# Kernel tuning notes

Measured on AMD Instinct MI355X. Metric: run time of the kernel, lower is better.

Reference implementation:

```python
import jax, jax.numpy as jnp
import numpy as np

PAD = 0  # padding_index
BIG = 10000.0

B, S = 1024, 128
V, E, H, T = 200, 512, 512, 24


def setup_inputs() -> dict:
    key = jax.random.key(0)
    ks = jax.random.split(key, 12)
    sequences = jax.random.randint(ks[0], (B, S), 0, V, dtype=jnp.int32)
    labels = jax.random.randint(ks[1], (B, S), 0, T, dtype=jnp.int32)
    true_lengths = jax.random.randint(ks[2], (B,), 1, S, dtype=jnp.int32)
    emb = jax.random.normal(ks[3], (V, E), dtype=jnp.float32) * 0.1
    emb = emb.at[PAD].set(0.0)  # nn.Embedding padding_idx zeros that row
    w1 = jax.random.normal(ks[4], (H, H), dtype=jnp.float32) * (1.0 / np.sqrt(H))
    b1 = jax.random.normal(ks[5], (H,), dtype=jnp.float32) * 0.01
    w2 = jax.random.normal(ks[6], (T, H), dtype=jnp.float32) * (1.0 / np.sqrt(H))
    b2 = jax.random.normal(ks[7], (T,), dtype=jnp.float32) * 0.01
    start_trans = jax.random.uniform(ks[8], (T,), jnp.float32, -0.1, 0.1)
    end_trans = jax.random.uniform(ks[9], (T,), jnp.float32, -0.1, 0.1)
    transitions = jax.random.uniform(ks[10], (T, T), jnp.float32, -0.1, 0.1)
    return {"sequences": sequences, "labels": labels, "true_lengths": true_lengths,
            "emb": emb, "w1": w1, "b1": b1, "w2": w2, "b2": b2,
            "start_trans": start_trans, "end_trans": end_trans, "transitions": transitions}


def _emissions(sequences, emb, w1, b1, w2, b2):
    pad_mask = (sequences == PAD).astype(jnp.float32)  # [B,S]
    x = emb[sequences]                                  # [B,S,E]
    h = jax.nn.relu(x @ w1.T + b1)                      # [B,S,H]
    scores = jax.nn.relu(h @ w2.T + b2)                 # [B,S,T]
    scores = scores.at[:, :, PAD].add(pad_mask * BIG)
    return scores


def _crf_nll_mean(emissions, labels, start_trans, end_trans, transitions):
    # emissions [B,S,T], labels [B,S]; mask = all ones (none passed in forward)
    # numerator: score of gold path
    em_gold = jnp.take_along_axis(emissions, labels[..., None], axis=2)[..., 0]  # [B,S]
    num = (start_trans[labels[:, 0]]
           + em_gold.sum(axis=1)
           + transitions[labels[:, :-1], labels[:, 1:]].sum(axis=1)
           + end_trans[labels[:, -1]])  # [B]
    # denominator: forward algorithm via scan over time
    em_t = jnp.swapaxes(emissions, 0, 1)  # [S,B,T]
    alpha0 = start_trans[None, :] + em_t[0]  # [B,T]

    def step(alpha, emit):
        # alpha [B,T_prev], transitions [T_prev,T_next], emit [B,T_next]
        nxt = jax.nn.logsumexp(alpha[:, :, None] + transitions[None] + emit[:, None, :], axis=1)
        return nxt, None

    alpha, _ = jax.lax.scan(step, alpha0, em_t[1:])
    denom = jax.nn.logsumexp(alpha + end_trans[None, :], axis=1)  # [B]
    llh = num - denom
    return -jnp.mean(llh)


def reference(sequences, labels, true_lengths, emb, w1, b1, w2, b2,
              start_trans, end_trans, transitions):
    emissions = _emissions(sequences, emb, w1, b1, w2, b2)
    return _crf_nll_mean(emissions, labels, start_trans, end_trans, transitions)
```

## Files before the change

### kernel.cpp

```cpp
#include <hip/hip_runtime.h>
#include <math.h>

#define PAD_IDX 0
#define BIGV 10000.0f
constexpr int B_ = 1024, S_ = 128, V_ = 200, E_ = 512, H_ = 512, T_ = 24;

constexpr int OFF_H  = 262144;
constexpr int OFF_EM = 364544;
constexpr int OFF_W  = 369344;
constexpr int OFF_MX = 374144;
constexpr int OFF_GP = 374344;

typedef __attribute__((ext_vector_type(8)))  short    bf8frag;
typedef __attribute__((ext_vector_type(16))) float    facc16;
typedef __attribute__((ext_vector_type(4)))  unsigned u32x4;

__device__ __forceinline__ unsigned short f2bf(float f) {
    unsigned u = __float_as_uint(f);
    u += 0x7fffu + ((u >> 16) & 1u);
    return (unsigned short)(u >> 16);
}
__device__ __forceinline__ unsigned pkbf(float lo, float hi) {
    const unsigned a = __float_as_uint(lo), b = __float_as_uint(hi);
    return ((a + 0x8000u) >> 16) | ((b + 0x8000u) & 0xffff0000u);
}

__global__ __launch_bounds__(256) void transpose_kernel(
    const float* __restrict__ w1, unsigned short* __restrict__ w1Tb,
    float* __restrict__ out)
{
    __shared__ float tile[64][65];
    const int bi = blockIdx.x >> 3, bj = blockIdx.x & 7;
    const int tx = threadIdx.x & 63, r0 = (threadIdx.x >> 6) * 16;
    if (blockIdx.x == 0 && threadIdx.x == 0) out[0] = 0.f;
    #pragma unroll
    for (int m = 0; m < 16; ++m) {
        const int r = r0 + m;
        tile[r][tx] = w1[(size_t)(bi * 64 + r) * 512 + bj * 64 + tx];
    }
    __syncthreads();
    #pragma unroll
    for (int m = 0; m < 16; ++m) {
        const int r = r0 + m;
        w1Tb[(size_t)(bj * 64 + r) * 512 + bi * 64 + tx] = f2bf(tile[tx][r]);
    }
}

__global__ __launch_bounds__(256) void h_kernel(
    const float* __restrict__ emb, const unsigned short* __restrict__ w1Tb,
    const float* __restrict__ b1, float* __restrict__ h_ws)
{
    __shared__ float xi[2 * E_];
    __shared__ float part_s[4][64][8];
    const int pair = blockIdx.x >> 1, half = blockIdx.x & 1;
    const int v0 = pair * 2, v1 = v0 + 1;
    const int tid = threadIdx.x;
    {
        const float* __restrict__ x0 = emb + (size_t)v0 * E_;
        const float* __restrict__ x1 = emb + (size_t)v1 * E_;
        #pragma unroll
        for (int m = 0; m < 2; ++m) {
            const int k = tid + m * 256;
            xi[2 * k]     = x0[k];
            xi[2 * k + 1] = x1[k];
        }
    }
    __syncthreads();
    const int part = tid >> 6, quad = tid & 63;
    const int t0 = half * 256 + quad * 4, k0 = part * 128;
    float a0 = 0.f, a1 = 0.f, a2 = 0.f, a3 = 0.f;
    float c0 = 0.f, c1 = 0.f, c2 = 0.f, c3 = 0.f;
    const unsigned short* __restrict__ wp = w1Tb + (size_t)k0 * H_ + t0;
    const float2* __restrict__ xp = (const float2*)xi + k0;
    #pragma unroll 4
    for (int i = 0; i < 128; ++i) {
        const uint2 wu = *(const uint2*)(wp + (size_t)i * H_);
        const float2 x = xp[i];
        const float w0 = __uint_as_float(wu.x << 16);
        const float w1v = __uint_as_float(wu.x & 0xffff0000u);
        const float w2v = __uint_as_float(wu.y << 16);
        const float w3v = __uint_as_float(wu.y & 0xffff0000u);
        a0 = fmaf(w0,  x.x, a0); a1 = fmaf(w1v, x.x, a1);
        a2 = fmaf(w2v, x.x, a2); a3 = fmaf(w3v, x.x, a3);
        c0 = fmaf(w0,  x.y, c0); c1 = fmaf(w1v, x.y, c1);
        c2 = fmaf(w2v, x.y, c2); c3 = fmaf(w3v, x.y, c3);
    }
    part_s[part][quad][0] = a0; part_s[part][quad][1] = a1;
    part_s[part][quad][2] = a2; part_s[part][quad][3] = a3;
    part_s[part][quad][4] = c0; part_s[part][quad][5] = c1;
    part_s[part][quad][6] = c2; part_s[part][quad][7] = c3;
    __syncthreads();
    {
        const int q2 = tid >> 2, r0 = tid & 3;
        const float s0 = (part_s[0][q2][r0]     + part_s[1][q2][r0])
                       + (part_s[2][q2][r0]     + part_s[3][q2][r0]);
        const float s1 = (part_s[0][q2][r0 + 4] + part_s[1][q2][r0 + 4])
                       + (part_s[2][q2][r0 + 4] + part_s[3][q2][r0 + 4]);
        const int t = half * 256 + tid;
        const float bb = b1[t];
        h_ws[(size_t)v0 * H_ + t] = fmaxf(s0 + bb, 0.f);
        h_ws[(size_t)v1 * H_ + t] = fmaxf(s1 + bb, 0.f);
    }
}

__global__ __launch_bounds__(256) void emis_kernel(
    const float* __restrict__ h_ws, const float* __restrict__ w2,
    const float* __restrict__ b2, float* __restrict__ em_table,
    float* __restrict__ w_table, float* __restrict__ emax_arr)
{
    __shared__ float em_row[32];
    const int v = blockIdx.x;
    const int t = threadIdx.x;
    const int wave = t >> 6, lane = t & 63;
    const float* __restrict__ hrow = h_ws + (size_t)v * H_;
    for (int jj2 = 0; jj2 < 6; ++jj2) {
        const int jo = wave * 6 + jj2;
        float part = 0.f;
        #pragma unroll
        for (int m = 0; m < H_ / 64; ++m) {
            const int k = lane + m * 64;
            part = fmaf(hrow[k], w2[(size_t)jo * H_ + k], part);
        }
        #pragma unroll
        for (int off = 32; off; off >>= 1)
            part += __shfl_xor(part, off, 64);
        if (lane == 0) {
            float val = fmaxf(part + b2[jo], 0.f);
            if (v == 0 && jo == PAD_IDX) val += BIGV;
            em_row[jo] = val;
        }
    }
    __syncthreads();
    if (t < 32) {
        float x = (t < T_) ? em_row[t] : -INFINITY;
        float mx = x;
        #pragma unroll
        for (int off = 16; off; off >>= 1)
            mx = fmaxf(mx, __shfl_xor(mx, off, 32));
        if (t < T_) {
            em_table[v * T_ + t] = x;
            w_table[v * T_ + t]  = __expf(x - mx);
        }
        if (t == 0) emax_arr[v] = mx;
    }
}

__global__ __launch_bounds__(256) void gold_kernel(
    const int* __restrict__ seq, const int* __restrict__ labels,
    const float* __restrict__ start_t, const float* __restrict__ end_t,
    const float* __restrict__ trans, const float* __restrict__ em_table,
    const float* __restrict__ emax_arr, float* __restrict__ gp_ws)
{
    const int grp = threadIdx.x >> 5, j = threadIdx.x & 31;
    const int b = blockIdx.x * 8 + grp;
    const int* __restrict__ srow = seq + (size_t)b * S_;
    const int* __restrict__ lrow = labels + (size_t)b * S_;
    float gp = 0.f;
    #pragma unroll
    for (int r = 0; r < 4; ++r) {
        const int s = j + r * 32;
        const int tk = srow[s], ls = lrow[s];
        gp += em_table[tk * T_ + ls];
        if (s >= 1) gp -= emax_arr[tk];
        if (s < S_ - 1) gp += trans[ls * T_ + lrow[s + 1]];
        if (s == 0) gp += start_t[ls];
        if (s == S_ - 1) gp += end_t[ls];
    }
    #pragma unroll
    for (int off = 16; off; off >>= 1)
        gp += __shfl_xor(gp, off, 32);
    if (j == 0) gp_ws[b] = gp;
}

__global__ __launch_bounds__(128) void crf_kernel(
    const int* __restrict__ seq,
    const float* __restrict__ start_t, const float* __restrict__ end_t,
    const float* __restrict__ trans, const float* __restrict__ em_table,
    const float* __restrict__ w_table, const float* __restrict__ gp_ws,
    float* __restrict__ out)
{
    __shared__ __align__(16) float w_s[V_ * T_];
    __shared__ int   tok_s[S_ * 32];
    __shared__ float meet_s[64 * 12];
    __shared__ float logb_s[64];
    const int tid = threadIdx.x;
    const int g = blockIdx.x;

    for (int i = tid; i < V_ * T_ / 4; i += 128)
        ((float4*)w_s)[i] = ((const float4*)w_table)[i];
    {
        const int bq = tid & 31, c = tid >> 5;
        const int* __restrict__ src = seq + (size_t)(g * 32 + bq) * S_ + c * 32;
        #pragma unroll 4
        for (int i = 0; i < 32; ++i)
            tok_s[(c * 32 + i) * 32 + bq] = src[i];
    }
    __syncthreads();

    const bool isF = (tid < 64);
    const int lane = tid & 63;
    const int n = lane & 31;
    const int h = lane >> 5;

    u32x4 A1p, A2p;
    {
        float a1e[8], a2e[8];
        #pragma unroll
        for (int j = 0; j < 8; ++j) {
            const int k1 = 8 * h + j;
            const int k2 = 16 + 8 * h + j;
            float v1 = 0.f, v2 = 0.f;
            if (n < T_) {
                v1 = __expf(isF ? trans[k1 * T_ + n] : trans[n * T_ + k1]);
                if (k2 < T_)
                    v2 = __expf(isF ? trans[k2 * T_ + n] : trans[n * T_ + k2]);
            }
            a1e[j] = v1; a2e[j] = v2;
        }
        #pragma unroll
        for (int r = 0; r < 4; ++r) {
            A1p[r] = pkbf(a1e[2 * r], a1e[2 * r + 1]);
            A2p[r] = pkbf(a2e[2 * r], a2e[2 * r + 1]);
        }
    }

    float logacc;
    u32x4 B1p, B2p;
    {
        const int tokI = tok_s[(isF ? 0 : (S_ - 1)) * 32 + n];
        float q1[8], q2[8];
        if (isF) {
            float e1[8], e2[8];
            #pragma unroll
            for (int j = 0; j < 8; ++j) { e1[j] = 0.f; e2[j] = 0.f; }
            float mx = -INFINITY;
            #pragma unroll
            for (int j = 0; j < 8; ++j) {
                const int r1 = 8 * h + j;
                e1[j] = start_t[r1] + em_table[tokI * T_ + r1];
                mx = fmaxf(mx, e1[j]);
            }
            if (h == 0) {
                #pragma unroll
                for (int j = 0; j < 8; ++j) {
                    const int r2 = 16 + j;
                    e2[j] = start_t[r2] + em_table[tokI * T_ + r2];
                    mx = fmaxf(mx, e2[j]);
                }
            }
            mx = fmaxf(mx, __shfl_xor(mx, 32, 64));
            #pragma unroll
            for (int j = 0; j < 8; ++j) {
                q1[j] = __expf(e1[j] - mx);
                q2[j] = (h == 0) ? __expf(e2[j] - mx) : 0.f;
            }
            logacc = mx;
        } else {
            #pragma unroll
            for (int j = 0; j < 8; ++j) {
                const int r1 = 8 * h + j;
                q1[j] = w_s[tokI * T_ + r1] * __expf(end_t[r1]);
                const int r2 = 16 + j;
                q2[j] = (h == 0) ? w_s[tokI * T_ + r2] * __expf(end_t[r2]) : 0.f;
            }
            logacc = 0.f;
        }
        #pragma unroll
        for (int r = 0; r < 4; ++r) {
            B1p[r] = pkbf(q1[2 * r], q1[2 * r + 1]);
            B2p[r] = pkbf(q2[2 * r], q2[2 * r + 1]);
        }
    }

    const int dir  = isF ? 1 : -1;
    const int offi = isF ? 1 : (S_ - 2);

    float4 Wc0, Wc1, Wc2;
    {
        const int tk = tok_s[offi * 32 + n];
        const float* wb = w_s + tk * T_ + 4 * h;
        Wc0 = *(const float4*)(wb);
        Wc1 = *(const float4*)(wb + 8);
        Wc2 = *(const float4*)(wb + 16);
    }

    float d[12];
    for (int s = 1; s <= 63; ++s) {
        const int sn = (s < 63) ? (s + 1) : 63;
        const int tkN = tok_s[(offi + dir * (sn - 1)) * 32 + n];
        const float* wbn = w_s + tkN * T_ + 4 * h;
        const float4 Wn0 = *(const float4*)(wbn);
        const float4 Wn1 = *(const float4*)(wbn + 8);
        const float4 Wn2 = *(const float4*)(wbn + 16);

        facc16 acc;
        #pragma unroll
        for (int r = 0; r < 16; ++r) acc[r] = 0.f;
        acc = __builtin_amdgcn_mfma_f32_32x32x16_bf16(
                  __builtin_bit_cast(bf8frag, A2p),
                  __builtin_bit_cast(bf8frag, B2p), acc, 0, 0, 0);
        acc = __builtin_amdgcn_mfma_f32_32x32x16_bf16(
                  __builtin_bit_cast(bf8frag, A1p),
                  __builtin_bit_cast(bf8frag, B1p), acc, 0, 0, 0);

        d[0] = acc[0]*Wc0.x;  d[1] = acc[1]*Wc0.y;  d[2]  = acc[2]*Wc0.z;  d[3]  = acc[3]*Wc0.w;
        d[4] = acc[4]*Wc1.x;  d[5] = acc[5]*Wc1.y;  d[6]  = acc[6]*Wc1.z;  d[7]  = acc[7]*Wc1.w;
        d[8] = acc[8]*Wc2.x;  d[9] = acc[9]*Wc2.y;  d[10] = acc[10]*Wc2.z; d[11] = acc[11]*Wc2.w;

        if ((s & 15) == 0 || s == 63) {
            float mx = d[0];
            #pragma unroll
            for (int r = 1; r < 12; ++r) mx = fmaxf(mx, d[r]);
            mx = fmaxf(mx, __shfl_xor(mx, 32, 64));
            const float inv = 1.0f / mx;
            #pragma unroll
            for (int r = 0; r < 12; ++r) d[r] *= inv;
            logacc += __logf(mx);
        }

        const unsigned P0 = pkbf(d[0], d[1]),  P1 = pkbf(d[2], d[3]);
        const unsigned P2 = pkbf(d[4], d[5]),  P3 = pkbf(d[6], d[7]);
        const unsigned P4 = pkbf(d[8], d[9]),  P5 = pkbf(d[10], d[11]);
        const unsigned XP0 = (unsigned)__shfl_xor((int)P0, 32, 64);
        const unsigned XP1 = (unsigned)__shfl_xor((int)P1, 32, 64);
        const unsigned XP2 = (unsigned)__shfl_xor((int)P2, 32, 64);
        const unsigned XP3 = (unsigned)__shfl_xor((int)P3, 32, 64);
        const unsigned XP4 = (unsigned)__shfl_xor((int)P4, 32, 64);
        const unsigned XP5 = (unsigned)__shfl_xor((int)P5, 32, 64);
        B1p[0] = h ? XP2 : P0;  B1p[1] = h ? XP3 : P1;
        B1p[2] = h ? P2  : XP0; B1p[3] = h ? P3  : XP1;
        B2p[0] = h ? 0u  : P4;  B2p[1] = h ? 0u  : P5;
        B2p[2] = h ? 0u  : XP4; B2p[3] = h ? 0u  : XP5;

        Wc0 = Wn0; Wc1 = Wn1; Wc2 = Wn2;
    }

    if (!isF) {
        #pragma unroll
        for (int r = 0; r < 12; ++r) meet_s[lane * 12 + r] = d[r];
        logb_s[lane] = logacc;
    }
    __syncthreads();
    if (isF) {
        facc16 acc;
        #pragma unroll
        for (int r = 0; r < 16; ++r) acc[r] = 0.f;
        acc = __builtin_amdgcn_mfma_f32_32x32x16_bf16(
                  __builtin_bit_cast(bf8frag, A2p),
                  __builtin_bit_cast(bf8frag, B2p), acc, 0, 0, 0);
        acc = __builtin_amdgcn_mfma_f32_32x32x16_bf16(
                  __builtin_bit_cast(bf8frag, A1p),
                  __builtin_bit_cast(bf8frag, B1p), acc, 0, 0, 0);
        float dot = 0.f;
        #pragma unroll
        for (int r = 0; r < 12; ++r)
            dot = fmaf(acc[r], meet_s[lane * 12 + r], dot);
        dot += __shfl_xor(dot, 32, 64);
        const float denom = logacc + logb_s[lane] + __logf(dot);
        float val = 0.f;
        if (h == 0)
            val = (denom - gp_ws[g * 32 + n]) * (1.0f / (float)B_);
        #pragma unroll
        for (int off = 32; off; off >>= 1)
            val += __shfl_xor(val, off, 64);
        if (lane == 0) atomicAdd(out, val);
    }
}

extern "C" void kernel_launch(void* const* d_in, const int* in_sizes, int n_in,
                              void* d_out, int out_size, void* d_ws, size_t ws_size,
                              hipStream_t stream) {
    const int*   seq     = (const int*)d_in[0];
    const int*   labels  = (const int*)d_in[1];
    const float* emb     = (const float*)d_in[3];
    const float* w1      = (const float*)d_in[4];
    const float* b1      = (const float*)d_in[5];
    const float* w2      = (const float*)d_in[6];
    const float* b2      = (const float*)d_in[7];
    const float* start_t = (const float*)d_in[8];
    const float* end_t   = (const float*)d_in[9];
    const float* trans   = (const float*)d_in[10];

    float* ws       = (float*)d_ws;
    unsigned short* w1Tb = (unsigned short*)d_ws;
    float* h_ws     = ws + OFF_H;
    float* em_table = ws + OFF_EM;
    float* w_table  = ws + OFF_W;
    float* emax_arr = ws + OFF_MX;
    float* gp_ws    = ws + OFF_GP;
    float* out      = (float*)d_out;

    transpose_kernel<<<64, 256, 0, stream>>>(w1, w1Tb, out);
    h_kernel<<<200, 256, 0, stream>>>(emb, w1Tb, b1, h_ws);
    emis_kernel<<<V_, 256, 0, stream>>>(h_ws, w2, b2, em_table, w_table, emax_arr);
    gold_kernel<<<B_ / 8, 256, 0, stream>>>(seq, labels, start_t, end_t, trans,
                                            em_table, emax_arr, gp_ws);
    crf_kernel<<<B_ / 32, 128, 0, stream>>>(seq, start_t, end_t, trans,
                                            em_table, w_table, gp_ws, out);
}
```

Measured before the change: 119.6 us.

## Fuse MLP kernels and merge gold-path scoring into CRF kernel

Merges the hidden-layer and emission kernels into one mlp_kernel, where each block handles two vocab rows and keeps h in shared memory instead of a global workspace. The gold-path score kernel becomes two extra waves inside the CRF kernel: they accumulate per-sequence scores into shared memory with atomics while the forward/backward waves run their recurrence. This cuts the launch count from five to three and drops the global round trips for h and the gold scores. In exchange the MLP phase runs on half as many blocks with longer per-block loops, and correctness depends on the __syncthreads calls in the two divergent branches pairing up.

```diff
diff --git a/kernel.cpp b/kernel.cpp
--- a/kernel.cpp
+++ b/kernel.cpp
@@ -5,11 +5,9 @@
 #define BIGV 10000.0f
 constexpr int B_ = 1024, S_ = 128, V_ = 200, E_ = 512, H_ = 512, T_ = 24;
 
-constexpr int OFF_H  = 262144;
-constexpr int OFF_EM = 364544;
-constexpr int OFF_W  = 369344;
-constexpr int OFF_MX = 374144;
-constexpr int OFF_GP = 374344;
+constexpr int OFF_EM = 262144;
+constexpr int OFF_W  = 267008;
+constexpr int OFF_MX = 271872;
 
 typedef __attribute__((ext_vector_type(8)))  short    bf8frag;
 typedef __attribute__((ext_vector_type(16))) float    facc16;
@@ -46,15 +44,19 @@
     }
 }
 
-__global__ __launch_bounds__(256) void h_kernel(
+__global__ __launch_bounds__(256) void mlp_kernel(
     const float* __restrict__ emb, const unsigned short* __restrict__ w1Tb,
-    const float* __restrict__ b1, float* __restrict__ h_ws)
+    const float* __restrict__ b1, const float* __restrict__ w2,
+    const float* __restrict__ b2, float* __restrict__ em_table,
+    float* __restrict__ w_table, float* __restrict__ emax_arr)
 {
     __shared__ float xi[2 * E_];
-    __shared__ float part_s[4][64][8];
-    const int pair = blockIdx.x >> 1, half = blockIdx.x & 1;
-    const int v0 = pair * 2, v1 = v0 + 1;
+    __shared__ float part_s[2][128][8];
+    __shared__ float hs[2][H_];
+    __shared__ float em_row[2][32];
+    const int v0 = blockIdx.x * 2, v1 = v0 + 1;
     const int tid = threadIdx.x;
+
     {
         const float* __restrict__ x0 = emb + (size_t)v0 * E_;
         const float* __restrict__ x1 = emb + (size_t)v1 * E_;
@@ -66,304 +68,303 @@
         }
     }
     __syncthreads();
-    const int part = tid >> 6, quad = tid & 63;
-    const int t0 = half * 256 + quad * 4, k0 = part * 128;
-    float a0 = 0.f, a1 = 0.f, a2 = 0.f, a3 = 0.f;
-    float c0 = 0.f, c1 = 0.f, c2 = 0.f, c3 = 0.f;
-    const unsigned short* __restrict__ wp = w1Tb + (size_t)k0 * H_ + t0;
-    const float2* __restrict__ xp = (const float2*)xi + k0;
-    #pragma unroll 4
-    for (int i = 0; i < 128; ++i) {
-        const uint2 wu = *(const uint2*)(wp + (size_t)i * H_);
-        const float2 x = xp[i];
-        const float w0 = __uint_as_float(wu.x << 16);
-        const float w1v = __uint_as_float(wu.x & 0xffff0000u);
-        const float w2v = __uint_as_float(wu.y << 16);
-        const float w3v = __uint_as_float(wu.y & 0xffff0000u);
-        a0 = fmaf(w0,  x.x, a0); a1 = fmaf(w1v, x.x, a1);
-        a2 = fmaf(w2v, x.x, a2); a3 = fmaf(w3v, x.x, a3);
-        c0 = fmaf(w0,  x.y, c0); c1 = fmaf(w1v, x.y, c1);
-        c2 = fmaf(w2v, x.y, c2); c3 = fmaf(w3v, x.y, c3);
-    }
-    part_s[part][quad][0] = a0; part_s[part][quad][1] = a1;
-    part_s[part][quad][2] = a2; part_s[part][quad][3] = a3;
-    part_s[part][quad][4] = c0; part_s[part][quad][5] = c1;
-    part_s[part][quad][6] = c2; part_s[part][quad][7] = c3;
-    __syncthreads();
-    {
-        const int q2 = tid >> 2, r0 = tid & 3;
-        const float s0 = (part_s[0][q2][r0]     + part_s[1][q2][r0])
-                       + (part_s[2][q2][r0]     + part_s[3][q2][r0]);
-        const float s1 = (part_s[0][q2][r0 + 4] + part_s[1][q2][r0 + 4])
-                       + (part_s[2][q2][r0 + 4] + part_s[3][q2][r0 + 4]);
-        const int t = half * 256 + tid;
-        const float bb = b1[t];
-        h_ws[(size_t)v0 * H_ + t] = fmaxf(s0 + bb, 0.f);
-        h_ws[(size_t)v1 * H_ + t] = fmaxf(s1 + bb, 0.f);
-    }
-}
-
-__global__ __launch_bounds__(256) void emis_kernel(
-    const float* __restrict__ h_ws, const float* __restrict__ w2,
-    const float* __restrict__ b2, float* __restrict__ em_table,
-    float* __restrict__ w_table, float* __restrict__ emax_arr)
-{
-    __shared__ float em_row[32];
-    const int v = blockIdx.x;
-    const int t = threadIdx.x;
-    const int wave = t >> 6, lane = t & 63;
-    const float* __restrict__ hrow = h_ws + (size_t)v * H_;
-    for (int jj2 = 0; jj2 < 6; ++jj2) {
-        const int jo = wave * 6 + jj2;
-        float part = 0.f;
+
+    {
+        const int part = tid >> 7;
+        const int tq   = tid & 127;
+        const int t0 = tq * 4, k0 = part * 256;
+        float a0 = 0.f, a1 = 0.f, a2 = 0.f, a3 = 0.f;
+        float c0 = 0.f, c1 = 0.f, c2 = 0.f, c3 = 0.f;
+        const unsigned short* __restrict__ wp = w1Tb + (size_t)k0 * H_ + t0;
+        const float2* __restrict__ xp = (const float2*)xi + k0;
+        #pragma unroll 4
+        for (int i = 0; i < 256; ++i) {
+            const uint2 wu = *(const uint2*)(wp + (size_t)i * H_);
+            const float2 x = xp[i];
+            const float w0 = __uint_as_float(wu.x << 16);
+            const float w1v = __uint_as_float(wu.x & 0xffff0000u);
+            const float w2v = __uint_as_float(wu.y << 16);
+            const float w3v = __uint_as_float(wu.y & 0xffff0000u);
+            a0 = fmaf(w0,  x.x, a0); a1 = fmaf(w1v, x.x, a1);
+            a2 = fmaf(w2v, x.x, a2); a3 = fmaf(w3v, x.x, a3);
+            c0 = fmaf(w0,  x.y, c0); c1 = fmaf(w1v, x.y, c1);
+            c2 = fmaf(w2v, x.y, c2); c3 = fmaf(w3v, x.y, c3);
+        }
+        part_s[part][tq][0] = a0; part_s[part][tq][1] = a1;
+        part_s[part][tq][2] = a2; part_s[part][tq][3] = a3;
+        part_s[part][tq][4] = c0; part_s[part][tq][5] = c1;
+        part_s[part][tq][6] = c2; part_s[part][tq][7] = c3;
+    }
+    __syncthreads();
+    {
         #pragma unroll
-        for (int m = 0; m < H_ / 64; ++m) {
-            const int k = lane + m * 64;
-            part = fmaf(hrow[k], w2[(size_t)jo * H_ + k], part);
-        }
-        #pragma unroll
-        for (int off = 32; off; off >>= 1)
-            part += __shfl_xor(part, off, 64);
-        if (lane == 0) {
-            float val = fmaxf(part + b2[jo], 0.f);
-            if (v == 0 && jo == PAD_IDX) val += BIGV;
-            em_row[jo] = val;
-        }
-    }
-    __syncthreads();
-    if (t < 32) {
-        float x = (t < T_) ? em_row[t] : -INFINITY;
+        for (int m = 0; m < 2; ++m) {
+            const int t = tid + m * 256;
+            const int q2 = t >> 2, r = t & 3;
+            const float s0 = part_s[0][q2][r]     + part_s[1][q2][r];
+            const float s1 = part_s[0][q2][r + 4] + part_s[1][q2][r + 4];
+            const float bb = b1[t];
+            hs[0][t] = fmaxf(s0 + bb, 0.f);
+            hs[1][t] = fmaxf(s1 + bb, 0.f);
+        }
+    }
+    __syncthreads();
+
+    {
+        const int wave = tid >> 6, lane = tid & 63;
+        const int vsel = wave >> 1;
+        const float* __restrict__ hrow = hs[vsel];
+        for (int jj2 = 0; jj2 < 12; ++jj2) {
+            const int j = (wave & 1) * 12 + jj2;
+            float part = 0.f;
+            #pragma unroll
+            for (int m = 0; m < H_ / 64; ++m) {
+                const int k = lane + m * 64;
+                part = fmaf(hrow[k], w2[(size_t)j * H_ + k], part);
+            }
+            #pragma unroll
+            for (int off = 32; off; off >>= 1)
+                part += __shfl_xor(part, off, 64);
+            if (lane == 0) {
+                float val = fmaxf(part + b2[j], 0.f);
+                if (v0 == 0 && vsel == 0 && j == PAD_IDX) val += BIGV;
+                em_row[vsel][j] = val;
+            }
+        }
+    }
+    __syncthreads();
+
+    if (tid < 64) {
+        const int grp = tid >> 5, j = tid & 31;
+        const int v = v0 + grp;
+        float x = (j < T_) ? em_row[grp][j] : -INFINITY;
         float mx = x;
         #pragma unroll
         for (int off = 16; off; off >>= 1)
             mx = fmaxf(mx, __shfl_xor(mx, off, 32));
-        if (t < T_) {
-            em_table[v * T_ + t] = x;
-            w_table[v * T_ + t]  = __expf(x - mx);
-        }
-        if (t == 0) emax_arr[v] = mx;
-    }
-}
-
-__global__ __launch_bounds__(256) void gold_kernel(
+        if (j < T_) {
+            em_table[v * T_ + j] = x;
+            w_table[v * T_ + j]  = __expf(x - mx);
+        }
+        if (j == 0) emax_arr[v] = mx;
+    }
+}
+
+__global__ __launch_bounds__(256) void crf_kernel(
     const int* __restrict__ seq, const int* __restrict__ labels,
     const float* __restrict__ start_t, const float* __restrict__ end_t,
     const float* __restrict__ trans, const float* __restrict__ em_table,
-    const float* __restrict__ emax_arr, float* __restrict__ gp_ws)
-{
-    const int grp = threadIdx.x >> 5, j = threadIdx.x & 31;
-    const int b = blockIdx.x * 8 + grp;
-    const int* __restrict__ srow = seq + (size_t)b * S_;
-    const int* __restrict__ lrow = labels + (size_t)b * S_;
-    float gp = 0.f;
-    #pragma unroll
-    for (int r = 0; r < 4; ++r) {
-        const int s = j + r * 32;
-        const int tk = srow[s], ls = lrow[s];
-        gp += em_table[tk * T_ + ls];
-        if (s >= 1) gp -= emax_arr[tk];
-        if (s < S_ - 1) gp += trans[ls * T_ + lrow[s + 1]];
-        if (s == 0) gp += start_t[ls];
-        if (s == S_ - 1) gp += end_t[ls];
-    }
-    #pragma unroll
-    for (int off = 16; off; off >>= 1)
-        gp += __shfl_xor(gp, off, 32);
-    if (j == 0) gp_ws[b] = gp;
-}
-
-__global__ __launch_bounds__(128) void crf_kernel(
-    const int* __restrict__ seq,
-    const float* __restrict__ start_t, const float* __restrict__ end_t,
-    const float* __restrict__ trans, const float* __restrict__ em_table,
-    const float* __restrict__ w_table, const float* __restrict__ gp_ws,
+    const float* __restrict__ w_table, const float* __restrict__ emax_arr,
     float* __restrict__ out)
 {
     __shared__ __align__(16) float w_s[V_ * T_];
     __shared__ int   tok_s[S_ * 32];
     __shared__ float meet_s[64 * 12];
     __shared__ float logb_s[64];
+    __shared__ float gp_s[32];
     const int tid = threadIdx.x;
     const int g = blockIdx.x;
 
-    for (int i = tid; i < V_ * T_ / 4; i += 128)
+    for (int i = tid; i < V_ * T_ / 4; i += 256)
         ((float4*)w_s)[i] = ((const float4*)w_table)[i];
     {
         const int bq = tid & 31, c = tid >> 5;
-        const int* __restrict__ src = seq + (size_t)(g * 32 + bq) * S_ + c * 32;
-        #pragma unroll 4
-        for (int i = 0; i < 32; ++i)
-            tok_s[(c * 32 + i) * 32 + bq] = src[i];
-    }
-    __syncthreads();
-
-    const bool isF = (tid < 64);
-    const int lane = tid & 63;
-    const int n = lane & 31;
-    const int h = lane >> 5;
-
-    u32x4 A1p, A2p;
-    {
-        float a1e[8], a2e[8];
+        const int* __restrict__ src = seq + (size_t)(g * 32 + bq) * S_ + c * 16;
         #pragma unroll
-        for (int j = 0; j < 8; ++j) {
-            const int k1 = 8 * h + j;
-            const int k2 = 16 + 8 * h + j;
-            float v1 = 0.f, v2 = 0.f;
-            if (n < T_) {
-                v1 = __expf(isF ? trans[k1 * T_ + n] : trans[n * T_ + k1]);
-                if (k2 < T_)
-                    v2 = __expf(isF ? trans[k2 * T_ + n] : trans[n * T_ + k2]);
-            }
-            a1e[j] = v1; a2e[j] = v2;
-        }
-        #pragma unroll
-        for (int r = 0; r < 4; ++r) {
-            A1p[r] = pkbf(a1e[2 * r], a1e[2 * r + 1]);
-            A2p[r] = pkbf(a2e[2 * r], a2e[2 * r + 1]);
-        }
-    }
-
-    float logacc;
-    u32x4 B1p, B2p;
-    {
-        const int tokI = tok_s[(isF ? 0 : (S_ - 1)) * 32 + n];
-        float q1[8], q2[8];
+        for (int i = 0; i < 16; ++i)
+            tok_s[(c * 16 + i) * 32 + bq] = src[i];
+    }
+    if (tid < 32) gp_s[tid] = 0.f;
+    __syncthreads();
+
+    if (tid < 128) {
+        const bool isF = (tid < 64);
+        const int lane = tid & 63;
+        const int n = lane & 31;
+        const int h = lane >> 5;
+
+        u32x4 A1p, A2p;
+        {
+            float a1e[8], a2e[8];
+            #pragma unroll
+            for (int j = 0; j < 8; ++j) {
+                const int k1 = 8 * h + j;
+                const int k2 = 16 + 8 * h + j;
+                float v1 = 0.f, v2 = 0.f;
+                if (n < T_) {
+                    v1 = __expf(isF ? trans[k1 * T_ + n] : trans[n * T_ + k1]);
+                    if (k2 < T_)
+                        v2 = __expf(isF ? trans[k2 * T_ + n] : trans[n * T_ + k2]);
+                }
+                a1e[j] = v1; a2e[j] = v2;
+            }
+            #pragma unroll
+            for (int r = 0; r < 4; ++r) {
+                A1p[r] = pkbf(a1e[2 * r], a1e[2 * r + 1]);
+                A2p[r] = pkbf(a2e[2 * r], a2e[2 * r + 1]);
+            }
+        }
+
+        float logacc;
+        u32x4 B1p, B2p;
+        {
+            const int tokI = tok_s[(isF ? 0 : (S_ - 1)) * 32 + n];
+            float q1[8], q2[8];
+            if (isF) {
+                float e1[8], e2[8];
+                #pragma unroll
+                for (int j = 0; j < 8; ++j) { e1[j] = 0.f; e2[j] = 0.f; }
+                float mx = -INFINITY;
+                #pragma unroll
+                for (int j = 0; j < 8; ++j) {
+                    const int r1 = 8 * h + j;
+                    e1[j] = start_t[r1] + em_table[tokI * T_ + r1];
+                    mx = fmaxf(mx, e1[j]);
+                }
+                if (h == 0) {
+                    #pragma unroll
+                    for (int j = 0; j < 8; ++j) {
+                        const int r2 = 16 + j;
+                        e2[j] = start_t[r2] + em_table[tokI * T_ + r2];
+                        mx = fmaxf(mx, e2[j]);
+                    }
+                }
+                mx = fmaxf(mx, __shfl_xor(mx, 32, 64));
+                #pragma unroll
+                for (int j = 0; j < 8; ++j) {
+                    q1[j] = __expf(e1[j] - mx);
+                    q2[j] = (h == 0) ? __expf(e2[j] - mx) : 0.f;
+                }
+                logacc = mx;
+            } else {
+                #pragma unroll
+                for (int j = 0; j < 8; ++j) {
+                    const int r1 = 8 * h + j;
+                    q1[j] = w_s[tokI * T_ + r1] * __expf(end_t[r1]);
+                    const int r2 = 16 + j;
+                    q2[j] = (h == 0) ? w_s[tokI * T_ + r2] * __expf(end_t[r2]) : 0.f;
+                }
+                logacc = 0.f;
+            }
+            #pragma unroll
+            for (int r = 0; r < 4; ++r) {
+                B1p[r] = pkbf(q1[2 * r], q1[2 * r + 1]);
+                B2p[r] = pkbf(q2[2 * r], q2[2 * r + 1]);
+            }
+        }
+
+        const int dir  = isF ? 1 : -1;
+        const int offi = isF ? 1 : (S_ - 2);
+
+        float4 Wc0, Wc1, Wc2;
+        {
+            const int tk = tok_s[offi * 32 + n];
+            const float* wb = w_s + tk * T_ + 4 * h;
+            Wc0 = *(const float4*)(wb);
+            Wc1 = *(const float4*)(wb + 8);
+            Wc2 = *(const float4*)(wb + 16);
+        }
+
+        float d[12];
+        for (int s = 1; s <= 63; ++s) {
+            const int sn = (s < 63) ? (s + 1) : 63;
+            const int tkN = tok_s[(offi + dir * (sn - 1)) * 32 + n];
+            const float* wbn = w_s + tkN * T_ + 4 * h;
+            const float4 Wn0 = *(const float4*)(wbn);
+            const float4 Wn1 = *(const float4*)(wbn + 8);
+            const float4 Wn2 = *(const float4*)(wbn + 16);
+
+            facc16 acc;
+            #pragma unroll
+            for (int r = 0; r < 16; ++r) acc[r] = 0.f;
+            acc = __builtin_amdgcn_mfma_f32_32x32x16_bf16(
+                      __builtin_bit_cast(bf8frag, A2p),
+                      __builtin_bit_cast(bf8frag, B2p), acc, 0, 0, 0);
+            acc = __builtin_amdgcn_mfma_f32_32x32x16_bf16(
+                      __builtin_bit_cast(bf8frag, A1p),
+                      __builtin_bit_cast(bf8frag, B1p), acc, 0, 0, 0);
+
+            d[0] = acc[0]*Wc0.x;  d[1] = acc[1]*Wc0.y;  d[2]  = acc[2]*Wc0.z;  d[3]  = acc[3]*Wc0.w;
+            d[4] = acc[4]*Wc1.x;  d[5] = acc[5]*Wc1.y;  d[6]  = acc[6]*Wc1.z;  d[7]  = acc[7]*Wc1.w;
+            d[8] = acc[8]*Wc2.x;  d[9] = acc[9]*Wc2.y;  d[10] = acc[10]*Wc2.z; d[11] = acc[11]*Wc2.w;
+
+            if ((s & 15) == 0 || s == 63) {
+                float mx = d[0];
+                #pragma unroll
+                for (int r = 1; r < 12; ++r) mx = fmaxf(mx, d[r]);
+                mx = fmaxf(mx, __shfl_xor(mx, 32, 64));
+                const float inv = 1.0f / mx;
+                #pragma unroll
+                for (int r = 0; r < 12; ++r) d[r] *= inv;
+                logacc += __logf(mx);
+            }
+
+            const unsigned P0 = pkbf(d[0], d[1]),  P1 = pkbf(d[2], d[3]);
+            const unsigned P2 = pkbf(d[4], d[5]),  P3 = pkbf(d[6], d[7]);
+            const unsigned P4 = pkbf(d[8], d[9]),  P5 = pkbf(d[10], d[11]);
+            const unsigned XP0 = (unsigned)__shfl_xor((int)P0, 32, 64);
+            const unsigned XP1 = (unsigned)__shfl_xor((int)P1, 32, 64);
+            const unsigned XP2 = (unsigned)__shfl_xor((int)P2, 32, 64);
+            const unsigned XP3 = (unsigned)__shfl_xor((int)P3, 32, 64);
+            const unsigned XP4 = (unsigned)__shfl_xor((int)P4, 32, 64);
+            const unsigned XP5 = (unsigned)__shfl_xor((int)P5, 32, 64);
+            B1p[0] = h ? XP2 : P0;  B1p[1] = h ? XP3 : P1;
+            B1p[2] = h ? P2  : XP0; B1p[3] = h ? P3  : XP1;
+            B2p[0] = h ? 0u  : P4;  B2p[1] = h ? 0u  : P5;
+            B2p[2] = h ? 0u  : XP4; B2p[3] = h ? 0u  : XP5;
+
+            Wc0 = Wn0; Wc1 = Wn1; Wc2 = Wn2;
+        }
+
+        if (!isF) {
+            #pragma unroll
+            for (int r = 0; r < 12; ++r) meet_s[lane * 12 + r] = d[r];
+            logb_s[lane] = logacc;
+        }
+        __syncthreads();
         if (isF) {
-            float e1[8], e2[8];
-            #pragma unroll
-            for (int j = 0; j < 8; ++j) { e1[j] = 0.f; e2[j] = 0.f; }
-            float mx = -INFINITY;
-            #pragma unroll
-            for (int j = 0; j < 8; ++j) {
-                const int r1 = 8 * h + j;
-                e1[j] = start_t[r1] + em_table[tokI * T_ + r1];
-                mx = fmaxf(mx, e1[j]);
-            }
-            if (h == 0) {
-                #pragma unroll
-                for (int j = 0; j < 8; ++j) {
-                    const int r2 = 16 + j;
-                    e2[j] = start_t[r2] + em_table[tokI * T_ + r2];
-                    mx = fmaxf(mx, e2[j]);
-                }
-            }
-            mx = fmaxf(mx, __shfl_xor(mx, 32, 64));
-            #pragma unroll
-            for (int j = 0; j < 8; ++j) {
-                q1[j] = __expf(e1[j] - mx);
-                q2[j] = (h == 0) ? __expf(e2[j] - mx) : 0.f;
-            }
-            logacc = mx;
-        } else {
-            #pragma unroll
-            for (int j = 0; j < 8; ++j) {
-                const int r1 = 8 * h + j;
-                q1[j] = w_s[tokI * T_ + r1] * __expf(end_t[r1]);
-                const int r2 = 16 + j;
-                q2[j] = (h == 0) ? w_s[tokI * T_ + r2] * __expf(end_t[r2]) : 0.f;
-            }
-            logacc = 0.f;
-        }
-        #pragma unroll
-        for (int r = 0; r < 4; ++r) {
-            B1p[r] = pkbf(q1[2 * r], q1[2 * r + 1]);
-            B2p[r] = pkbf(q2[2 * r], q2[2 * r + 1]);
-        }
-    }
-
-    const int dir  = isF ? 1 : -1;
-    const int offi = isF ? 1 : (S_ - 2);
-
-    float4 Wc0, Wc1, Wc2;
-    {
-        const int tk = tok_s[offi * 32 + n];
-        const float* wb = w_s + tk * T_ + 4 * h;
-        Wc0 = *(const float4*)(wb);
-        Wc1 = *(const float4*)(wb + 8);
-        Wc2 = *(const float4*)(wb + 16);
-    }
-
-    float d[12];
-    for (int s = 1; s <= 63; ++s) {
-        const int sn = (s < 63) ? (s + 1) : 63;
-        const int tkN = tok_s[(offi + dir * (sn - 1)) * 32 + n];
-        const float* wbn = w_s + tkN * T_ + 4 * h;
-        const float4 Wn0 = *(const float4*)(wbn);
-        const float4 Wn1 = *(const float4*)(wbn + 8);
-        const float4 Wn2 = *(const float4*)(wbn + 16);
-
-        facc16 acc;
-        #pragma unroll
-        for (int r = 0; r < 16; ++r) acc[r] = 0.f;
-        acc = __builtin_amdgcn_mfma_f32_32x32x16_bf16(
-                  __builtin_bit_cast(bf8frag, A2p),
-                  __builtin_bit_cast(bf8frag, B2p), acc, 0, 0, 0);
-        acc = __builtin_amdgcn_mfma_f32_32x32x16_bf16(
-                  __builtin_bit_cast(bf8frag, A1p),
-                  __builtin_bit_cast(bf8frag, B1p), acc, 0, 0, 0);
-
-        d[0] = acc[0]*Wc0.x;  d[1] = acc[1]*Wc0.y;  d[2]  = acc[2]*Wc0.z;  d[3]  = acc[3]*Wc0.w;
-        d[4] = acc[4]*Wc1.x;  d[5] = acc[5]*Wc1.y;  d[6]  = acc[6]*Wc1.z;  d[7]  = acc[7]*Wc1.w;
-        d[8] = acc[8]*Wc2.x;  d[9] = acc[9]*Wc2.y;  d[10] = acc[10]*Wc2.z; d[11] = acc[11]*Wc2.w;
-
-        if ((s & 15) == 0 || s == 63) {
-            float mx = d[0];
-            #pragma unroll
-            for (int r = 1; r < 12; ++r) mx = fmaxf(mx, d[r]);
-            mx = fmaxf(mx, __shfl_xor(mx, 32, 64));
-            const float inv = 1.0f / mx;
-            #pragma unroll
-            for (int r = 0; r < 12; ++r) d[r] *= inv;
-            logacc += __logf(mx);
-        }
-
-        const unsigned P0 = pkbf(d[0], d[1]),  P1 = pkbf(d[2], d[3]);
-        const unsigned P2 = pkbf(d[4], d[5]),  P3 = pkbf(d[6], d[7]);
-        const unsigned P4 = pkbf(d[8], d[9]),  P5 = pkbf(d[10], d[11]);
-        const unsigned XP0 = (unsigned)__shfl_xor((int)P0, 32, 64);
-        const unsigned XP1 = (unsigned)__shfl_xor((int)P1, 32, 64);
-        const unsigned XP2 = (unsigned)__shfl_xor((int)P2, 32, 64);
-        const unsigned XP3 = (unsigned)__shfl_xor((int)P3, 32, 64);
-        const unsigned XP4 = (unsigned)__shfl_xor((int)P4, 32, 64);
-        const unsigned XP5 = (unsigned)__shfl_xor((int)P5, 32, 64);
-        B1p[0] = h ? XP2 : P0;  B1p[1] = h ? XP3 : P1;
-        B1p[2] = h ? P2  : XP0; B1p[3] = h ? P3  : XP1;
-        B2p[0] = h ? 0u  : P4;  B2p[1] = h ? 0u  : P5;
-        B2p[2] = h ? 0u  : XP4; B2p[3] = h ? 0u  : XP5;
-
-        Wc0 = Wn0; Wc1 = Wn1; Wc2 = Wn2;
-    }
-
-    if (!isF) {
-        #pragma unroll
-        for (int r = 0; r < 12; ++r) meet_s[lane * 12 + r] = d[r];
-        logb_s[lane] = logacc;
-    }
-    __syncthreads();
-    if (isF) {
-        facc16 acc;
-        #pragma unroll
-        for (int r = 0; r < 16; ++r) acc[r] = 0.f;
-        acc = __builtin_amdgcn_mfma_f32_32x32x16_bf16(
-                  __builtin_bit_cast(bf8frag, A2p),
-                  __builtin_bit_cast(bf8frag, B2p), acc, 0, 0, 0);
-        acc = __builtin_amdgcn_mfma_f32_32x32x16_bf16(
-                  __builtin_bit_cast(bf8frag, A1p),
-                  __builtin_bit_cast(bf8frag, B1p), acc, 0, 0, 0);
-        float dot = 0.f;
-        #pragma unroll
-        for (int r = 0; r < 12; ++r)
-            dot = fmaf(acc[r], meet_s[lane * 12 + r], dot);
-        dot += __shfl_xor(dot, 32, 64);
-        const float denom = logacc + logb_s[lane] + __logf(dot);
-        float val = 0.f;
-        if (h == 0)
-            val = (denom - gp_ws[g * 32 + n]) * (1.0f / (float)B_);
-        #pragma unroll
-        for (int off = 32; off; off >>= 1)
-            val += __shfl_xor(val, off, 64);
-        if (lane == 0) atomicAdd(out, val);
+            facc16 acc;
+            #pragma unroll
+            for (int r = 0; r < 16; ++r) acc[r] = 0.f;
+            acc = __builtin_amdgcn_mfma_f32_32x32x16_bf16(
+                      __builtin_bit_cast(bf8frag, A2p),
+                      __builtin_bit_cast(bf8frag, B2p), acc, 0, 0, 0);
+            acc = __builtin_amdgcn_mfma_f32_32x32x16_bf16(
+                      __builtin_bit_cast(bf8frag, A1p),
+                      __builtin_bit_cast(bf8frag, B1p), acc, 0, 0, 0);
+            float dot = 0.f;
+            #pragma unroll
+            for (int r = 0; r < 12; ++r)
+                dot = fmaf(acc[r], meet_s[lane * 12 + r], dot);
+            dot += __shfl_xor(dot, 32, 64);
+            const float denom = logacc + logb_s[lane] + __logf(dot);
+            float val = 0.f;
+            if (h == 0)
+                val = (denom - gp_s[n]) * (1.0f / (float)B_);
+            #pragma unroll
+            for (int off = 32; off; off >>= 1)
+                val += __shfl_xor(val, off, 64);
+            if (lane == 0) atomicAdd(out, val);
+        }
+    } else {
+        const int t2 = tid - 128;
+        const int n = t2 & 31;
+        const int r = t2 >> 5;
+        const int b = g * 32 + n;
+        const int* __restrict__ lrow = labels + (size_t)b * S_;
+        float gp = 0.f;
+        for (int i = 0; i < 32; ++i) {
+            const int s = r * 32 + i;
+            const int tk = tok_s[s * 32 + n];
+            const int ls = lrow[s];
+            gp += em_table[tk * T_ + ls];
+            if (s >= 1) gp -= emax_arr[tk];
+            if (s < S_ - 1) gp += trans[ls * T_ + lrow[s + 1]];
+            if (s == 0) gp += start_t[ls];
+            if (s == S_ - 1) gp += end_t[ls];
+        }
+        atomicAdd(&gp_s[n], gp);
+        __syncthreads();
     }
 }
 
@@ -381,20 +382,16 @@
     const float* end_t   = (const float*)d_in[9];
     const float* trans   = (const float*)d_in[10];
 
-    float* ws       = (float*)d_ws;
+    float* ws            = (float*)d_ws;
     unsigned short* w1Tb = (unsigned short*)d_ws;
-    float* h_ws     = ws + OFF_H;
-    float* em_table = ws + OFF_EM;
-    float* w_table  = ws + OFF_W;
-    float* emax_arr = ws + OFF_MX;
-    float* gp_ws    = ws + OFF_GP;
-    float* out      = (float*)d_out;
+    float* em_table      = ws + OFF_EM;
+    float* w_table       = ws + OFF_W;
+    float* emax_arr      = ws + OFF_MX;
+    float* out           = (float*)d_out;
 
     transpose_kernel<<<64, 256, 0, stream>>>(w1, w1Tb, out);
-    h_kernel<<<200, 256, 0, stream>>>(emb, w1Tb, b1, h_ws);
-    emis_kernel<<<V_, 256, 0, stream>>>(h_ws, w2, b2, em_table, w_table, emax_arr);
-    gold_kernel<<<B_ / 8, 256, 0, stream>>>(seq, labels, start_t, end_t, trans,
-                                            em_table, emax_arr, gp_ws);
-    crf_kernel<<<B_ / 32, 128, 0, stream>>>(seq, start_t, end_t, trans,
-                                            em_table, w_table, gp_ws, out);
-}
+    mlp_kernel<<<V_ / 2, 256, 0, stream>>>(emb, w1Tb, b1, w2, b2,
+                                           em_table, w_table, emax_arr);
+    crf_kernel<<<B_ / 32, 256, 0, stream>>>(seq, labels, start_t, end_t, trans,
+                                            em_table, w_table, emax_arr, out);
+}
```

Result: slower. 124.5 us (+4.2%).
